# Kernel optimization log

Hardware: AMD Instinct MI355X
Metric: run time of the kernel (lower is better)

## Reference

```python
import jax, jax.numpy as jnp
import numpy as np

N_HEAD = 16
N_EMBD = 1024
HEAD_DIM = N_EMBD // N_HEAD  # 64
ROPE_BASE = 10000.0


def _rotary_cos_sin(T, dim, dtype=jnp.float32):
    # matches Rotary: inv_freq over even indices, cos/sin cached in bfloat16
    inv_freq = 1.0 / (ROPE_BASE ** (jnp.arange(0, dim, 2, dtype=jnp.float32) / dim))
    freqs = jnp.arange(T, dtype=jnp.float32)[:, None] * inv_freq[None, :]  # [T, dim/2]
    cos = jnp.cos(freqs).astype(jnp.bfloat16).astype(dtype)
    sin = jnp.sin(freqs).astype(jnp.bfloat16).astype(dtype)
    # shape [1, T, 1, dim/2] to broadcast over (B, T, H, d)
    return cos[None, :, None, :], sin[None, :, None, :]


def _apply_rotary(x, cos, sin):
    d = x.shape[3] // 2
    x1, x2 = x[..., :d], x[..., d:]
    y1 = x1 * cos + x2 * sin
    y2 = -x1 * sin + x2 * cos
    return jnp.concatenate([y1, y2], axis=3).astype(x.dtype)


def setup_inputs() -> dict:
    key = jax.random.key(0)
    ks = jax.random.split(key, 8)
    B, T, C = 2, 2048, N_EMBD
    scale = C ** -0.5  # realistic linear-layer init scale
    x = jax.random.normal(ks[0], (B, T, C), dtype=jnp.float32)
    Wq1 = jax.random.normal(ks[1], (C, C), dtype=jnp.float32) * scale
    Wk1 = jax.random.normal(ks[2], (C, C), dtype=jnp.float32) * scale
    Wq2 = jax.random.normal(ks[3], (C, C), dtype=jnp.float32) * scale
    Wk2 = jax.random.normal(ks[4], (C, C), dtype=jnp.float32) * scale
    Wv = jax.random.normal(ks[5], (C, C), dtype=jnp.float32) * scale
    Wout = jax.random.normal(ks[6], (C, C), dtype=jnp.float32) * scale
    return {"x": x, "Wq1": Wq1, "Wk1": Wk1, "Wq2": Wq2, "Wk2": Wk2, "Wv": Wv, "Wout": Wout}


def reference(x, Wq1, Wk1, Wq2, Wk2, Wv, Wout):
    B, T, C = x.shape
    H, D = N_HEAD, HEAD_DIM

    def proj(W):
        # torch nn.Linear(bias=False): y = x @ W.T
        return (x @ W.T).reshape(B, T, H, D)

    q1, k1 = proj(Wq1), proj(Wk1)
    q2, k2 = proj(Wq2), proj(Wk2)
    v = proj(Wv)

    cos, sin = _rotary_cos_sin(T, D, x.dtype)
    q1, k1 = _apply_rotary(q1, cos, sin), _apply_rotary(k1, cos, sin)
    q2, k2 = _apply_rotary(q2, cos, sin), _apply_rotary(k2, cos, sin)

    # two bilinear score maps, elementwise product, causal mask
    s1 = jnp.einsum('bqhd,bkhd->bhqk', q1, k1)  # [B,H,T,T]
    s2 = jnp.einsum('bqhd,bkhd->bhqk', q2, k2)
    causal = jnp.tril(jnp.ones((T, T), dtype=bool))
    pattern = jnp.where(causal[None, None], (s1 / D) * (s2 / D), 0.0)

    y = jnp.einsum('bhqk,bkhd->bqhd', pattern, v).reshape(B, T, C)
    return y @ Wout.T
```

## Files before the change

kernel.cpp:

```cpp
#include <hip/hip_runtime.h>
#include <hip/hip_bf16.h>
#include <math.h>

typedef __bf16 bf16;
typedef __bf16 bf16x8 __attribute__((ext_vector_type(8)));
typedef float  f32x4  __attribute__((ext_vector_type(4)));

#define NB    2
#define NT    2048
#define NH    16
#define ND    64
#define NC    1024
#define NBT   4096
#define NQT   32

#define AS1C(p) ((const __attribute__((address_space(1))) void*)(p))
#define AS3(p)  ((__attribute__((address_space(3))) void*)(p))

#define MFMA(a,b,c) __builtin_amdgcn_mfma_f32_16x16x32_bf16(a, b, c, 0, 0, 0)

__global__ void cast_kernel(const float* __restrict__ src, bf16* __restrict__ dst, int n)
{
    int i = (blockIdx.x * blockDim.x + threadIdx.x) * 4;
    if (i + 3 < n) {
        float4 v = *reinterpret_cast<const float4*>(src + i);
        dst[i+0] = (bf16)v.x;
        dst[i+1] = (bf16)v.y;
        dst[i+2] = (bf16)v.z;
        dst[i+3] = (bf16)v.w;
    }
}

struct WPtrs { const float* p[6]; };
__global__ void cast6_kernel(WPtrs w, bf16* __restrict__ dst)
{
    const int mat = blockIdx.x >> 10;
    const int off = ((blockIdx.x & 1023) * 256 + threadIdx.x) * 4;
    float4 v = *reinterpret_cast<const float4*>(w.p[mat] + off);
    bf16* d = dst + (size_t)mat * NC * NC + off;
    d[0] = (bf16)v.x; d[1] = (bf16)v.y; d[2] = (bf16)v.z; d[3] = (bf16)v.w;
}

__global__ void rope_table_kernel(float2* __restrict__ tbl)
{
    int i = blockIdx.x * 256 + threadIdx.x;
    int t = i >> 5, j = i & 31;
    float invf = 1.0f / powf(10000.0f, (float)j * (1.0f/32.0f));
    float fr = (float)t * invf;
    float2 cs;
    cs.x = (float)(bf16)cosf(fr);
    cs.y = (float)(bf16)sinf(fr);
    tbl[i] = cs;
}

__global__ __launch_bounds__(512, 1)
void gemm_proj(const bf16* __restrict__ A, const bf16* __restrict__ Bw,
               bf16* __restrict__ qkv, const float2* __restrict__ tbl)
{
    __shared__ bf16 smem[2*32768];

    const int tid  = threadIdx.x;
    const int lane = tid & 63;
    const int w    = tid >> 6;
    const int wr   = w >> 2;
    const int wc   = w & 3;

    const int id  = blockIdx.x;
    const int swz = (id & 7) * 40 + (id >> 3);
    const int by  = swz / 20, bx = swz % 20;
    const int row0 = by * 256, col0 = bx * 256;

    const int lo  = lane & 15;
    const int hi  = lane >> 4;

    const int srow = tid >> 3;
    const int ssw  = ((tid & 7) ^ (srow & 7)) * 8;

    f32x4 acc[8][4] = {};

    auto stage = [&](int buf, int kt) {
        char* As = (char*)smem + buf*65536;
        char* Bs = As + 32768;
        #pragma unroll
        for (int i = 0; i < 4; ++i) {
            const unsigned loff = (unsigned)(i*8192 + w*1024);
            __builtin_amdgcn_global_load_lds(
                AS1C(A + (size_t)(row0 + i*64 + srow) * NC + kt + ssw),
                AS3(As + loff), 16, 0, 0);
            __builtin_amdgcn_global_load_lds(
                AS1C(Bw + (size_t)(col0 + i*64 + srow) * NC + kt + ssw),
                AS3(Bs + loff), 16, 0, 0);
        }
    };

    stage(0, 0);
    asm volatile("s_waitcnt vmcnt(0)" ::: "memory");
    __syncthreads();

    for (int kt = 0; kt < 16; ++kt) {
        const int cur = kt & 1;
        if (kt < 15) stage(cur ^ 1, (kt + 1) * 64);

        const char* As = (const char*)smem + cur*65536;
        const char* Bs = As + 32768;

        __builtin_amdgcn_s_setprio(1);
        #pragma unroll
        for (int ks = 0; ks < 2; ++ks) {
            bf16x8 af[8], bfr[4];
            #pragma unroll
            for (int m = 0; m < 8; ++m) {
                const int ar = wr*128 + m*16 + lo;
                af[m] = *reinterpret_cast<const bf16x8*>(
                    As + ar*128 + (((ks*4 + hi) ^ (lo & 7)) * 16));
            }
            #pragma unroll
            for (int n = 0; n < 4; ++n) {
                const int br = wc*64 + n*16 + lo;
                bfr[n] = *reinterpret_cast<const bf16x8*>(
                    Bs + br*128 + (((ks*4 + hi) ^ (lo & 7)) * 16));
            }
            #pragma unroll
            for (int m = 0; m < 8; ++m)
                #pragma unroll
                for (int n = 0; n < 4; ++n)
                    acc[m][n] = MFMA(af[m], bfr[n], acc[m][n]);
        }
        __builtin_amdgcn_s_setprio(0);

        asm volatile("s_waitcnt vmcnt(0)" ::: "memory");
        __syncthreads();
    }

    bf16* Ct = smem;
    const int p  = col0 >> 10;
    const int h0 = (col0 >> 6) & (NH-1);
    const int rb = hi * 4;

    if (p < 4) {
        const float qsc = (p == 0 || p == 2) ? 0.015625f : 1.0f;
        #pragma unroll
        for (int m = 0; m < 8; ++m)
            #pragma unroll
            for (int r = 0; r < 4; ++r) {
                const int rl = wr*128 + m*16 + rb + r;
                const int t  = (row0 + rl) & (NT-1);
                const unsigned key = ((unsigned)(rl >> 2) & 3) << 5;
                #pragma unroll
                for (int n = 0; n < 2; ++n) {
                    const int j = n*16 + lo;
                    float2 cs = tbl[t*32 + j];
                    float a1 = acc[m][n][r];
                    float a2 = acc[m][n+2][r];
                    const int c1 = wc*64 + j;
                    const int c2 = c1 + 32;
                    *(bf16*)((char*)Ct + (unsigned)(rl*512 + (((unsigned)c1*2) ^ key)))
                        = (bf16)((a1*cs.x + a2*cs.y) * qsc);
                    *(bf16*)((char*)Ct + (unsigned)(rl*512 + (((unsigned)c2*2) ^ key)))
                        = (bf16)((a2*cs.x - a1*cs.y) * qsc);
                }
            }
        __syncthreads();
        #pragma unroll
        for (int it = 0; it < 16; ++it) {
            const int chunk = it*512 + tid;
            const int rl = chunk >> 5;
            const int cc = chunk & 31;
            const unsigned key = ((unsigned)(rl >> 2) & 3) << 5;
            bf16x8 val = *reinterpret_cast<const bf16x8*>(
                (const char*)Ct + (unsigned)(rl*512 + (((unsigned)cc*16) ^ key)));
            const int rowg = row0 + rl;
            const int b = rowg >> 11;
            const int t = rowg & (NT-1);
            const int hh = h0 + (cc >> 3);
            const int d  = (cc & 7) * 8;
            *reinterpret_cast<bf16x8*>(
                qkv + ((((size_t)p*NB + b)*NH + hh)*NT + t)*ND + d) = val;
        }
    } else {
        #pragma unroll
        for (int m = 0; m < 8; ++m)
            #pragma unroll
            for (int r = 0; r < 4; ++r) {
                const int rl = wr*128 + m*16 + rb + r;
                #pragma unroll
                for (int n = 0; n < 4; ++n) {
                    const int c = wc*64 + n*16 + lo;
                    *(bf16*)((char*)Ct + (unsigned)(c*512 + (((unsigned)rl*2) ^ ((c&7)<<4))))
                        = (bf16)acc[m][n][r];
                }
            }
        __syncthreads();
        const int b  = row0 >> 11;
        const int t0 = row0 & (NT-1);
        #pragma unroll
        for (int it = 0; it < 16; ++it) {
            const int chunk = it*512 + tid;
            const int c   = chunk >> 5;
            const int tcc = chunk & 31;
            bf16x8 val = *reinterpret_cast<const bf16x8*>(
                (const char*)Ct + (unsigned)(c*512 + (((unsigned)tcc*16) ^ ((c&7)<<4))));
            const int hh = h0 + (c >> 6);
            const int d  = c & 63;
            *reinterpret_cast<bf16x8*>(
                qkv + (((size_t)4*NB + b)*NH + hh)*(size_t)NT*ND
                    + (size_t)d*NT + t0 + tcc*8) = val;
        }
    }
}

__global__ __launch_bounds__(256)
void gemm_out(const bf16* __restrict__ A, const bf16* __restrict__ Bw,
              float* __restrict__ Cp)
{
    __shared__ bf16 smem[2*16384];

    const int tid  = threadIdx.x;
    const int lane = tid & 63;
    const int w    = tid >> 6;
    const int wr   = w >> 1;
    const int wc   = w & 1;
    const int row0 = blockIdx.y * 128;
    const int col0 = blockIdx.x * 128;

    const int lo  = lane & 15;
    const int hi  = lane >> 4;

    const int srow = tid >> 3;
    const int ssw  = ((tid & 7) ^ (srow & 7)) * 8;

    f32x4 acc[4][4] = {};

    auto stage = [&](int buf, int kt) {
        char* As = (char*)smem + buf*32768;
        char* Bs = As + 16384;
        #pragma unroll
        for (int i = 0; i < 4; ++i) {
            const unsigned loff = (unsigned)(i*4096 + w*1024);
            __builtin_amdgcn_global_load_lds(
                AS1C(A + (size_t)(row0 + i*32 + srow) * NC + kt + ssw),
                AS3(As + loff), 16, 0, 0);
            __builtin_amdgcn_global_load_lds(
                AS1C(Bw + (size_t)(col0 + i*32 + srow) * NC + kt + ssw),
                AS3(Bs + loff), 16, 0, 0);
        }
    };

    stage(0, 0);
    asm volatile("s_waitcnt vmcnt(0)" ::: "memory");
    __syncthreads();

    for (int kt = 0; kt < 16; ++kt) {
        const int cur = kt & 1;
        if (kt < 15) stage(cur ^ 1, (kt + 1) * 64);

        const char* As = (const char*)smem + cur*32768;
        const char* Bs = As + 16384;

        __builtin_amdgcn_s_setprio(1);
        #pragma unroll
        for (int ks = 0; ks < 2; ++ks) {
            bf16x8 af[4], bfr[4];
            #pragma unroll
            for (int m = 0; m < 4; ++m) {
                const int ar = wr*64 + m*16 + lo;
                af[m] = *reinterpret_cast<const bf16x8*>(
                    As + ar*128 + (((ks*4 + hi) ^ (lo & 7)) * 16));
            }
            #pragma unroll
            for (int n = 0; n < 4; ++n) {
                const int br = wc*64 + n*16 + lo;
                bfr[n] = *reinterpret_cast<const bf16x8*>(
                    Bs + br*128 + (((ks*4 + hi) ^ (lo & 7)) * 16));
            }
            #pragma unroll
            for (int m = 0; m < 4; ++m)
                #pragma unroll
                for (int n = 0; n < 4; ++n)
                    acc[m][n] = MFMA(af[m], bfr[n], acc[m][n]);
        }
        __builtin_amdgcn_s_setprio(0);

        asm volatile("s_waitcnt vmcnt(0)" ::: "memory");
        __syncthreads();
    }

    const int rb = hi * 4;
    #pragma unroll
    for (int m = 0; m < 4; ++m)
        #pragma unroll
        for (int n = 0; n < 4; ++n)
            #pragma unroll
            for (int r = 0; r < 4; ++r) {
                int row = row0 + wr*64 + m*16 + rb + r;
                int col = col0 + wc*64 + n*16 + lo;
                Cp[(size_t)row * NC + col] = acc[m][n][r];
            }
}

__global__ __launch_bounds__(256, 2)
void attn_kernel(const bf16* __restrict__ qkv, bf16* __restrict__ Y)
{
    __shared__ bf16 K1s[2*4096];
    __shared__ bf16 K2s[2*4096];
    __shared__ bf16 Vts[2*4096];
    __shared__ bf16 Pa [4][1024];
    __shared__ bf16 Pb [4][1024];

    const int tid  = threadIdx.x;
    const int lane = tid & 63;
    const int w    = tid >> 6;

    const int lin  = blockIdx.x;
    const int xcd  = lin & 7;
    const int slot = lin >> 3;
    const int pair = xcd * 4 + (slot >> 4);
    const int qa   = slot & 15;
    const int h    = pair >> 1;
    const int b    = pair & 1;
    const int qb   = NQT - 1 - qa;

    const size_t plane = (size_t)NB * NH * NT * ND;
    const size_t bh    = ((size_t)b * NH + h) * (size_t)NT * ND;
    const bf16* Q1 = qkv + 0*plane + bh;
    const bf16* K1 = qkv + 1*plane + bh;
    const bf16* Q2 = qkv + 2*plane + bh;
    const bf16* K2 = qkv + 3*plane + bh;
    const bf16* V  = qkv + 4*plane + bh;

    const int lo  = lane & 15;
    const int hi  = lane >> 4;
    const int hi8 = hi * 8;

    bf16x8 q1fa[2], q2fa[2], q1fb[2], q2fb[2];
    #pragma unroll
    for (int dd = 0; dd < 2; ++dd) {
        const size_t ra  = (size_t)(qa*64 + w*16 + lo) * ND + dd*32 + hi8;
        const size_t rbq = (size_t)(qb*64 + w*16 + lo) * ND + dd*32 + hi8;
        q1fa[dd] = *reinterpret_cast<const bf16x8*>(Q1 + ra);
        q2fa[dd] = *reinterpret_cast<const bf16x8*>(Q2 + ra);
        q1fb[dd] = *reinterpret_cast<const bf16x8*>(Q1 + rbq);
        q2fb[dd] = *reinterpret_cast<const bf16x8*>(Q2 + rbq);
    }

    f32x4 yacca[4] = {}, yaccb[4] = {};

    const int srow = tid >> 3;
    const int ssw  = ((tid & 7) ^ (srow & 7)) * 8;

    auto stageK = [&](int buf, int k0) {
        #pragma unroll
        for (int i = 0; i < 2; ++i) {
            const unsigned loff = (unsigned)(buf*8192 + i*4096 + w*1024);
            __builtin_amdgcn_global_load_lds(
                AS1C(K1 + (size_t)(k0 + i*32 + srow) * ND + ssw),
                AS3((char*)K1s + loff), 16, 0, 0);
            __builtin_amdgcn_global_load_lds(
                AS1C(K2 + (size_t)(k0 + i*32 + srow) * ND + ssw),
                AS3((char*)K2s + loff), 16, 0, 0);
        }
    };
    auto stageVT = [&](int buf, int k0) {
        #pragma unroll
        for (int i = 0; i < 2; ++i) {
            const int inst = w*2 + i;
            const int d    = inst*8 + (lane >> 3);
            const int sc   = ((lane & 7) ^ ((lane >> 3) & 7)) * 8;
            __builtin_amdgcn_global_load_lds(
                AS1C(V + (size_t)d * NT + k0 + sc),
                AS3((char*)Vts + (unsigned)(buf*8192 + inst*1024)), 16, 0, 0);
        }
    };

    stageK(0, 0);
    stageVT(0, 0);
    asm volatile("s_waitcnt vmcnt(0)" ::: "memory");
    __syncthreads();

    for (int kt = 0; kt <= qb; ++kt) {
        const int  cur = kt & 1;
        const bool pre = (kt < qb);
        const bool doA = (kt <= qa);
        const int  k0  = kt * 64;

        if (pre) { stageK(cur^1, k0 + 64); stageVT(cur^1, k0 + 64); }

        const bf16* K1b = K1s + cur*4096;
        const bf16* K2b = K2s + cur*4096;

        f32x4 s1a[4] = {}, s2a[4] = {}, s1b[4] = {}, s2b[4] = {};
        __builtin_amdgcn_s_setprio(1);
        #pragma unroll
        for (int dd = 0; dd < 2; ++dd)
            #pragma unroll
            for (int sub = 0; sub < 4; ++sub) {
                const unsigned kb = (unsigned)((sub*16 + lo)*128 + (((dd*4 + hi) ^ (lo & 7)) * 16));
                bf16x8 k1f = *reinterpret_cast<const bf16x8*>((const char*)K1b + kb);
                bf16x8 k2f = *reinterpret_cast<const bf16x8*>((const char*)K2b + kb);
                s1b[sub] = MFMA(q1fb[dd], k1f, s1b[sub]);
                s2b[sub] = MFMA(q2fb[dd], k2f, s2b[sub]);
                if (doA) {
                    s1a[sub] = MFMA(q1fa[dd], k1f, s1a[sub]);
                    s2a[sub] = MFMA(q2fa[dd], k2f, s2a[sub]);
                }
            }
        __builtin_amdgcn_s_setprio(0);

        #define COMBINE(S1, S2, PB, DIAG)                                              \
            _Pragma("unroll")                                                          \
            for (int sub = 0; sub < 4; ++sub)                                          \
                _Pragma("unroll")                                                      \
                for (int r = 0; r < 4; ++r) {                                          \
                    const int row = hi*4 + r;                                          \
                    const int col = sub*16 + lo;                                       \
                    const unsigned byte = (unsigned)(row*128 + (((col>>3) ^ (row&7))*16) + (col&7)*2); \
                    float pv = S1[sub][r] * S2[sub][r];                                \
                    if (DIAG && col > w*16 + row) pv = 0.0f;                           \
                    *(bf16*)((char*)PB + byte) = (bf16)pv;                             \
                }
        if (kt == qb) { COMBINE(s1b, s2b, Pb[w], true) } else { COMBINE(s1b, s2b, Pb[w], false) }
        if (doA) {
            if (kt == qa) { COMBINE(s1a, s2a, Pa[w], true) } else { COMBINE(s1a, s2a, Pa[w], false) }
        }
        #undef COMBINE

        asm volatile("s_waitcnt lgkmcnt(0)" ::: "memory");
        __builtin_amdgcn_sched_barrier(0);

        __builtin_amdgcn_s_setprio(1);
        #pragma unroll
        for (int ks = 0; ks < 2; ++ks) {
            const unsigned pby = (unsigned)(lo*128 + (((ks*4 + hi) ^ (lo & 7)) * 16));
            bf16x8 pfb = *reinterpret_cast<const bf16x8*>((const char*)Pb[w] + pby);
            bf16x8 pfa = {};
            if (doA) pfa = *reinterpret_cast<const bf16x8*>((const char*)Pa[w] + pby);
            #pragma unroll
            for (int n = 0; n < 4; ++n) {
                const unsigned vby = (unsigned)(cur*8192 + (n*16 + lo)*128 + (((ks*4 + hi) ^ (lo & 7)) * 16));
                bf16x8 vf = *reinterpret_cast<const bf16x8*>((const char*)Vts + vby);
                yaccb[n] = MFMA(pfb, vf, yaccb[n]);
                if (doA) yacca[n] = MFMA(pfa, vf, yacca[n]);
            }
        }
        __builtin_amdgcn_s_setprio(0);

        asm volatile("s_waitcnt vmcnt(0)" ::: "memory");
        __syncthreads();
    }

    auto writeOut = [&](int q0, const f32x4* ya, bf16* Pbuf) {
        #pragma unroll
        for (int n = 0; n < 4; ++n)
            #pragma unroll
            for (int r = 0; r < 4; ++r) {
                const int row = hi*4 + r;
                const int col = n*16 + lo;
                const unsigned byte = (unsigned)(row*128 + (((col>>3) ^ (row&7))*16) + (col&7)*2);
                *(bf16*)((char*)Pbuf + byte) = (bf16)ya[n][r];
            }
        asm volatile("s_waitcnt lgkmcnt(0)" ::: "memory");
        __builtin_amdgcn_sched_barrier(0);
        #pragma unroll
        for (int pass = 0; pass < 2; ++pass) {
            const int idx = pass*64 + lane;
            const int row = idx >> 3;
            const int cc  = idx & 7;
            bf16x8 val = *reinterpret_cast<const bf16x8*>(
                (const char*)Pbuf + row*128 + ((cc ^ (row&7))*16));
            const int t = q0 + w*16 + row;
            const int c = h*ND + cc*8;
            *reinterpret_cast<bf16x8*>(Y + ((size_t)b*NT + t)*NC + c) = val;
        }
    };
    writeOut(qa*64, yacca, Pa[w]);
    writeOut(qb*64, yaccb, Pb[w]);
}

extern "C" void kernel_launch(void* const* d_in, const int* in_sizes, int n_in,
                              void* d_out, int out_size, void* d_ws, size_t ws_size,
                              hipStream_t stream)
{
    const float* x = (const float*)d_in[0];

    char* ws = (char*)d_ws;
    bf16*   Xbf   = (bf16*)ws;
    bf16*   Wcat  = (bf16*)(ws + (size_t)NBT*NC*2);
    bf16*   QKV   = (bf16*)(ws + (size_t)NBT*NC*2 + (size_t)6*NC*NC*2);
    bf16*   Ybf   = (bf16*)((char*)QKV + (size_t)5*NBT*NC*2);
    float2* tbl   = (float2*)((char*)Ybf + (size_t)NBT*NC*2);
    bf16*   Woutb = Wcat + (size_t)5*NC*NC;

    cast_kernel<<<dim3(NBT*NC/1024), 256, 0, stream>>>(x, Xbf, NBT*NC);
    WPtrs wp;
    wp.p[0] = (const float*)d_in[1]; wp.p[1] = (const float*)d_in[2];
    wp.p[2] = (const float*)d_in[3]; wp.p[3] = (const float*)d_in[4];
    wp.p[4] = (const float*)d_in[5]; wp.p[5] = (const float*)d_in[6];
    cast6_kernel<<<dim3(6*1024), 256, 0, stream>>>(wp, Wcat);
    rope_table_kernel<<<dim3(NT*32/256), 256, 0, stream>>>(tbl);

    gemm_proj<<<dim3(320), 512, 0, stream>>>(Xbf, Wcat, QKV, tbl);
    attn_kernel<<<dim3(512), 256, 0, stream>>>(QKV, Ybf);
    gemm_out<<<dim3(NC/128, NBT/128), 256, 0, stream>>>(Ybf, Woutb, (float*)d_out);
}
```

Baseline: 161.6 us.

## Triple-buffer attention K/V staging, share P buffer, fuse prep kernels

Merges the x cast, the weight casts and the RoPE table build into one prep kernel, removing two launches. In the attention kernel, K1/K2/V tiles are now staged three deep: the loop waits only on the oldest load group (vmcnt(6)), so one barrier per iteration replaces the end-of-loop full drain. The two per-warp P buffers are merged into one, reused serially for the b and a query tiles, with V fragments held in registers for the second pass. This cuts shared memory per buffer set, but the serial P reuse adds extra lgkm waits and keeps more registers live.

```diff
diff --git a/kernel.cpp b/kernel.cpp
--- a/kernel.cpp
+++ b/kernel.cpp
@@ -19,38 +19,35 @@
 
 #define MFMA(a,b,c) __builtin_amdgcn_mfma_f32_16x16x32_bf16(a, b, c, 0, 0, 0)
 
-__global__ void cast_kernel(const float* __restrict__ src, bf16* __restrict__ dst, int n)
+struct WPtrs { const float* p[6]; };
+
+__global__ void prep_kernel(const float* __restrict__ x, WPtrs w,
+                            bf16* __restrict__ Xbf, bf16* __restrict__ Wcat,
+                            float2* __restrict__ tbl)
 {
-    int i = (blockIdx.x * blockDim.x + threadIdx.x) * 4;
-    if (i + 3 < n) {
-        float4 v = *reinterpret_cast<const float4*>(src + i);
-        dst[i+0] = (bf16)v.x;
-        dst[i+1] = (bf16)v.y;
-        dst[i+2] = (bf16)v.z;
-        dst[i+3] = (bf16)v.w;
+    const int bid = blockIdx.x;
+    if (bid < 4096) {
+        const int i = (bid * 256 + threadIdx.x) * 4;
+        float4 v = *reinterpret_cast<const float4*>(x + i);
+        Xbf[i+0] = (bf16)v.x; Xbf[i+1] = (bf16)v.y;
+        Xbf[i+2] = (bf16)v.z; Xbf[i+3] = (bf16)v.w;
+    } else if (bid < 10240) {
+        const int r   = bid - 4096;
+        const int mat = r >> 10;
+        const int off = ((r & 1023) * 256 + threadIdx.x) * 4;
+        float4 v = *reinterpret_cast<const float4*>(w.p[mat] + off);
+        bf16* d = Wcat + (size_t)mat * NC * NC + off;
+        d[0] = (bf16)v.x; d[1] = (bf16)v.y; d[2] = (bf16)v.z; d[3] = (bf16)v.w;
+    } else {
+        const int i = (bid - 10240) * 256 + threadIdx.x;
+        const int t = i >> 5, j = i & 31;
+        float invf = 1.0f / powf(10000.0f, (float)j * (1.0f/32.0f));
+        float fr = (float)t * invf;
+        float2 cs;
+        cs.x = (float)(bf16)cosf(fr);
+        cs.y = (float)(bf16)sinf(fr);
+        tbl[i] = cs;
     }
-}
-
-struct WPtrs { const float* p[6]; };
-__global__ void cast6_kernel(WPtrs w, bf16* __restrict__ dst)
-{
-    const int mat = blockIdx.x >> 10;
-    const int off = ((blockIdx.x & 1023) * 256 + threadIdx.x) * 4;
-    float4 v = *reinterpret_cast<const float4*>(w.p[mat] + off);
-    bf16* d = dst + (size_t)mat * NC * NC + off;
-    d[0] = (bf16)v.x; d[1] = (bf16)v.y; d[2] = (bf16)v.z; d[3] = (bf16)v.w;
-}
-
-__global__ void rope_table_kernel(float2* __restrict__ tbl)
-{
-    int i = blockIdx.x * 256 + threadIdx.x;
-    int t = i >> 5, j = i & 31;
-    float invf = 1.0f / powf(10000.0f, (float)j * (1.0f/32.0f));
-    float fr = (float)t * invf;
-    float2 cs;
-    cs.x = (float)(bf16)cosf(fr);
-    cs.y = (float)(bf16)sinf(fr);
-    tbl[i] = cs;
 }
 
 __global__ __launch_bounds__(512, 1)
@@ -301,11 +298,10 @@
 __global__ __launch_bounds__(256, 2)
 void attn_kernel(const bf16* __restrict__ qkv, bf16* __restrict__ Y)
 {
-    __shared__ bf16 K1s[2*4096];
-    __shared__ bf16 K2s[2*4096];
-    __shared__ bf16 Vts[2*4096];
-    __shared__ bf16 Pa [4][1024];
-    __shared__ bf16 Pb [4][1024];
+    __shared__ bf16 K1s[3*4096];
+    __shared__ bf16 K2s[3*4096];
+    __shared__ bf16 Vts[3*4096];
+    __shared__ bf16 Pl [4][1024];
 
     const int tid  = threadIdx.x;
     const int lane = tid & 63;
@@ -372,21 +368,24 @@
         }
     };
 
-    stageK(0, 0);
-    stageVT(0, 0);
-    asm volatile("s_waitcnt vmcnt(0)" ::: "memory");
-    __syncthreads();
-
+    stageK(0, 0);  stageVT(0, 0);
+    stageK(1, 64); stageVT(1, 64);
+
+    int cur = 0;
     for (int kt = 0; kt <= qb; ++kt) {
-        const int  cur = kt & 1;
-        const bool pre = (kt < qb);
+        if (kt < qb) asm volatile("s_waitcnt vmcnt(6)" ::: "memory");
+        else         asm volatile("s_waitcnt vmcnt(0)" ::: "memory");
+        __syncthreads();
+        if (kt + 2 <= qb) {
+            int nx = cur + 2; if (nx >= 3) nx -= 3;
+            stageK(nx, (kt + 2) * 64);
+            stageVT(nx, (kt + 2) * 64);
+        }
+
         const bool doA = (kt <= qa);
-        const int  k0  = kt * 64;
-
-        if (pre) { stageK(cur^1, k0 + 64); stageVT(cur^1, k0 + 64); }
-
         const bf16* K1b = K1s + cur*4096;
         const bf16* K2b = K2s + cur*4096;
+        const char* Vb  = (const char*)Vts + cur*8192;
 
         f32x4 s1a[4] = {}, s2a[4] = {}, s1b[4] = {}, s2b[4] = {};
         __builtin_amdgcn_s_setprio(1);
@@ -406,7 +405,7 @@
             }
         __builtin_amdgcn_s_setprio(0);
 
-        #define COMBINE(S1, S2, PB, DIAG)                                              \
+        #define COMBINE(S1, S2, DIAG)                                                  \
             _Pragma("unroll")                                                          \
             for (int sub = 0; sub < 4; ++sub)                                          \
                 _Pragma("unroll")                                                      \
@@ -416,39 +415,51 @@
                     const unsigned byte = (unsigned)(row*128 + (((col>>3) ^ (row&7))*16) + (col&7)*2); \
                     float pv = S1[sub][r] * S2[sub][r];                                \
                     if (DIAG && col > w*16 + row) pv = 0.0f;                           \
-                    *(bf16*)((char*)PB + byte) = (bf16)pv;                             \
+                    *(bf16*)((char*)Pl[w] + byte) = (bf16)pv;                          \
                 }
-        if (kt == qb) { COMBINE(s1b, s2b, Pb[w], true) } else { COMBINE(s1b, s2b, Pb[w], false) }
-        if (doA) {
-            if (kt == qa) { COMBINE(s1a, s2a, Pa[w], true) } else { COMBINE(s1a, s2a, Pa[w], false) }
-        }
-        #undef COMBINE
-
+
+        if (kt == qb) { COMBINE(s1b, s2b, true) } else { COMBINE(s1b, s2b, false) }
         asm volatile("s_waitcnt lgkmcnt(0)" ::: "memory");
         __builtin_amdgcn_sched_barrier(0);
 
+        bf16x8 vfr[2][4];
         __builtin_amdgcn_s_setprio(1);
         #pragma unroll
         for (int ks = 0; ks < 2; ++ks) {
             const unsigned pby = (unsigned)(lo*128 + (((ks*4 + hi) ^ (lo & 7)) * 16));
-            bf16x8 pfb = *reinterpret_cast<const bf16x8*>((const char*)Pb[w] + pby);
-            bf16x8 pfa = {};
-            if (doA) pfa = *reinterpret_cast<const bf16x8*>((const char*)Pa[w] + pby);
+            bf16x8 pfb = *reinterpret_cast<const bf16x8*>((const char*)Pl[w] + pby);
             #pragma unroll
             for (int n = 0; n < 4; ++n) {
-                const unsigned vby = (unsigned)(cur*8192 + (n*16 + lo)*128 + (((ks*4 + hi) ^ (lo & 7)) * 16));
-                bf16x8 vf = *reinterpret_cast<const bf16x8*>((const char*)Vts + vby);
-                yaccb[n] = MFMA(pfb, vf, yaccb[n]);
-                if (doA) yacca[n] = MFMA(pfa, vf, yacca[n]);
+                const unsigned vby = (unsigned)((n*16 + lo)*128 + (((ks*4 + hi) ^ (lo & 7)) * 16));
+                vfr[ks][n] = *reinterpret_cast<const bf16x8*>(Vb + vby);
+                yaccb[n] = MFMA(pfb, vfr[ks][n], yaccb[n]);
             }
         }
         __builtin_amdgcn_s_setprio(0);
 
-        asm volatile("s_waitcnt vmcnt(0)" ::: "memory");
-        __syncthreads();
+        if (doA) {
+            asm volatile("s_waitcnt lgkmcnt(0)" ::: "memory");
+            __builtin_amdgcn_sched_barrier(0);
+            if (kt == qa) { COMBINE(s1a, s2a, true) } else { COMBINE(s1a, s2a, false) }
+            asm volatile("s_waitcnt lgkmcnt(0)" ::: "memory");
+            __builtin_amdgcn_sched_barrier(0);
+            __builtin_amdgcn_s_setprio(1);
+            #pragma unroll
+            for (int ks = 0; ks < 2; ++ks) {
+                const unsigned pby = (unsigned)(lo*128 + (((ks*4 + hi) ^ (lo & 7)) * 16));
+                bf16x8 pfa = *reinterpret_cast<const bf16x8*>((const char*)Pl[w] + pby);
+                #pragma unroll
+                for (int n = 0; n < 4; ++n)
+                    yacca[n] = MFMA(pfa, vfr[ks][n], yacca[n]);
+            }
+            __builtin_amdgcn_s_setprio(0);
+        }
+        #undef COMBINE
+
+        cur += 1; if (cur >= 3) cur -= 3;
     }
 
-    auto writeOut = [&](int q0, const f32x4* ya, bf16* Pbuf) {
+    auto writeOut = [&](int q0, const f32x4* ya) {
         #pragma unroll
         for (int n = 0; n < 4; ++n)
             #pragma unroll
@@ -456,7 +467,7 @@
                 const int row = hi*4 + r;
                 const int col = n*16 + lo;
                 const unsigned byte = (unsigned)(row*128 + (((col>>3) ^ (row&7))*16) + (col&7)*2);
-                *(bf16*)((char*)Pbuf + byte) = (bf16)ya[n][r];
+                *(bf16*)((char*)Pl[w] + byte) = (bf16)ya[n][r];
             }
         asm volatile("s_waitcnt lgkmcnt(0)" ::: "memory");
         __builtin_amdgcn_sched_barrier(0);
@@ -466,14 +477,14 @@
             const int row = idx >> 3;
             const int cc  = idx & 7;
             bf16x8 val = *reinterpret_cast<const bf16x8*>(
-                (const char*)Pbuf + row*128 + ((cc ^ (row&7))*16));
+                (const char*)Pl[w] + row*128 + ((cc ^ (row&7))*16));
             const int t = q0 + w*16 + row;
             const int c = h*ND + cc*8;
             *reinterpret_cast<bf16x8*>(Y + ((size_t)b*NT + t)*NC + c) = val;
         }
     };
-    writeOut(qa*64, yacca, Pa[w]);
-    writeOut(qb*64, yaccb, Pb[w]);
+    writeOut(qa*64, yacca);
+    writeOut(qb*64, yaccb);
 }
 
 extern "C" void kernel_launch(void* const* d_in, const int* in_sizes, int n_in,
@@ -490,13 +501,12 @@
     float2* tbl   = (float2*)((char*)Ybf + (size_t)NBT*NC*2);
     bf16*   Woutb = Wcat + (size_t)5*NC*NC;
 
-    cast_kernel<<<dim3(NBT*NC/1024), 256, 0, stream>>>(x, Xbf, NBT*NC);
     WPtrs wp;
     wp.p[0] = (const float*)d_in[1]; wp.p[1] = (const float*)d_in[2];
     wp.p[2] = (const float*)d_in[3]; wp.p[3] = (const float*)d_in[4];
     wp.p[4] = (const float*)d_in[5]; wp.p[5] = (const float*)d_in[6];
-    cast6_kernel<<<dim3(6*1024), 256, 0, stream>>>(wp, Wcat);
-    rope_table_kernel<<<dim3(NT*32/256), 256, 0, stream>>>(tbl);
+
+    prep_kernel<<<dim3(10496), 256, 0, stream>>>(x, wp, Xbf, Wcat, tbl);
 
     gemm_proj<<<dim3(320), 512, 0, stream>>>(Xbf, Wcat, QKV, tbl);
     attn_kernel<<<dim3(512), 256, 0, stream>>>(QKV, Ybf);
```

After: 147.1 us. 1.1x faster.
